# Optimization experiments

Hardware: AMD Instinct MI355X
Metric: run time of the kernel (lower is better)

Reference implementation:

```python
import jax, jax.numpy as jnp
import numpy as np

T = 2048        # flattened tokens (one prefill sequence)
HID = 2048      # hidden_size
NH = 32         # query heads
NKV = 4         # kv heads
HD = 128        # head_dim
THETA = 1000000.0
EPS = 1e-6


def setup_inputs() -> dict:
    key = jax.random.key(0)
    k0, k1, k2 = jax.random.split(key, 3)
    return {
        "positions": jnp.arange(T, dtype=jnp.int32),
        "hidden_states": jax.random.normal(k0, (T, HID), dtype=jnp.float32),
        "w_qkv": jax.random.normal(k1, ((NH + 2 * NKV) * HD, HID), dtype=jnp.float32) * 0.02,
        "w_o": jax.random.normal(k2, (HID, NH * HD), dtype=jnp.float32) * 0.02,
        "q_norm_w": jnp.ones((HD,), dtype=jnp.float32),
        "k_norm_w": jnp.ones((HD,), dtype=jnp.float32),
    }


def _rmsnorm(x, w):
    # per-head RMSNorm over last dim (head_dim), fp32 math
    var = jnp.mean(x * x, axis=-1, keepdims=True)
    return x * jax.lax.rsqrt(var + EPS) * w


def _rope(x, positions):
    # NeoX-style rotary embedding over full head_dim
    d = x.shape[-1]
    inv_freq = 1.0 / (THETA ** (jnp.arange(0, d, 2, dtype=jnp.float32) / d))  # [d/2]
    ang = positions.astype(jnp.float32)[:, None] * inv_freq                   # [T, d/2]
    cos = jnp.cos(ang)[:, None, :]  # [T,1,d/2]
    sin = jnp.sin(ang)[:, None, :]
    x1, x2 = jnp.split(x, 2, axis=-1)
    return jnp.concatenate([x1 * cos - x2 * sin, x2 * cos + x1 * sin], axis=-1)


def reference(positions, hidden_states, w_qkv, w_o, q_norm_w, k_norm_w):
    # fused QKV projection (no bias)
    qkv = hidden_states @ w_qkv.T                       # [T, (NH+2*NKV)*HD]
    q, k, v = jnp.split(qkv, [NH * HD, (NH + NKV) * HD], axis=-1)
    q = _rmsnorm(q.reshape(T, NH, HD), q_norm_w)        # [T,NH,HD]
    k = _rmsnorm(k.reshape(T, NKV, HD), k_norm_w)       # [T,NKV,HD]
    v = v.reshape(T, NKV, HD)
    q = _rope(q, positions)
    k = _rope(k, positions)
    # GQA: expand kv heads to query heads
    g = NH // NKV
    k = jnp.repeat(k, g, axis=1)                        # [T,NH,HD]
    v = jnp.repeat(v, g, axis=1)
    scale = HD ** -0.5
    scores = jnp.einsum('qhd,khd->hqk', q, k) * scale   # [NH,T,T]
    causal = jnp.tril(jnp.ones((T, T), dtype=bool))
    scores = jnp.where(causal[None, :, :], scores, jnp.finfo(scores.dtype).min)
    attn = jax.nn.softmax(scores, axis=-1)
    o = jnp.einsum('hqk,khd->qhd', attn, v).reshape(T, NH * HD)
    return o @ w_o.T                                    # [T,HID]
```

## Files before the change

kernel.cpp:

```cpp
#include <hip/hip_runtime.h>
#include <math.h>

#define T 2048
#define HID 2048
#define NH 32
#define NKV 4
#define HD 128
#define QKV_DIM 5120
#define OD 4096
#define C2LOG 0.12751743f
#define MFIX 6.0f

typedef _Float16 half8 __attribute__((ext_vector_type(8)));
typedef _Float16 half4v __attribute__((ext_vector_type(4)));
typedef float floatx4 __attribute__((ext_vector_type(4)));
typedef float floatx16 __attribute__((ext_vector_type(16)));
typedef unsigned uint4v __attribute__((ext_vector_type(4)));

#define GLD16(gp, lp) __builtin_amdgcn_global_load_lds( \
    (const __attribute__((address_space(1))) void*)(gp), \
    (__attribute__((address_space(3))) void*)(lp), 16, 0, 0)

__device__ __forceinline__ unsigned pk_u32(float a, float b) {
    auto h = __builtin_amdgcn_cvt_pkrtz(a, b);
    return __builtin_bit_cast(unsigned, h);
}
__device__ __forceinline__ void plswap(unsigned &a, unsigned &b) {
    asm("v_permlane32_swap_b32 %0, %1" : "+v"(a), "+v"(b));
}

__global__ __launch_bounds__(256)
void cvt_all(const float* __restrict__ h, const float* __restrict__ wq,
             const float* __restrict__ wo, _Float16* __restrict__ out) {
    size_t i = ((size_t)blockIdx.x * 256 + threadIdx.x) * 4;
    const float* src;
    size_t off;
    if (i < (size_t)T * HID)                        { src = h;  off = i; }
    else if (i < (size_t)T * HID + (size_t)QKV_DIM * HID)
                                                    { src = wq; off = i - (size_t)T * HID; }
    else                                            { src = wo; off = i - (size_t)T * HID - (size_t)QKV_DIM * HID; }
    float4 v = *(const float4*)(src + off);
    half4v o = { (_Float16)v.x, (_Float16)v.y, (_Float16)v.z, (_Float16)v.w };
    *(half4v*)(out + i) = o;
}

__global__ __launch_bounds__(256)
void gemm_sk_h(const _Float16* __restrict__ A, const _Float16* __restrict__ B,
               _Float16* __restrict__ p0, _Float16* __restrict__ p1,
               int M, int N, int K, int KS) {
    __shared__ __align__(16) _Float16 Asm[8192];
    __shared__ __align__(16) _Float16 Bsm[8192];
    int tid = threadIdx.x;
    int wave = tid >> 6, lane = tid & 63;
    int quad = lane >> 4, l16 = lane & 15;
    int m0 = blockIdx.y * 128, n0 = blockIdx.x * 128;
    int koff = blockIdx.z * KS;
    _Float16* C = blockIdx.z ? p1 : p0;
    int wm = (wave >> 1) * 64, wn = (wave & 1) * 64;
    const _Float16* Ag = A + (size_t)(m0 + (tid >> 2)) * K + koff + (tid & 3) * 8;
    const _Float16* Bg = B + (size_t)(n0 + (tid >> 2)) * K + koff + (tid & 3) * 8;
    size_t row64 = (size_t)64 * K;
    int wofs = wave * 512;
    floatx4 acc[4][4] = {};
    int nt = KS >> 5;
    GLD16(Ag, Asm + wofs);
    GLD16(Ag + row64, Asm + 2048 + wofs);
    GLD16(Bg, Bsm + wofs);
    GLD16(Bg + row64, Bsm + 2048 + wofs);
    for (int t = 0; t < nt; t++) {
        int cur = t & 1;
        if (t + 1 < nt) {
            const _Float16* Agp = Ag + (size_t)(t + 1) * 32;
            const _Float16* Bgp = Bg + (size_t)(t + 1) * 32;
            int nb = (cur ^ 1) * 4096 + wofs;
            GLD16(Agp, Asm + nb);
            GLD16(Agp + row64, Asm + nb + 2048);
            GLD16(Bgp, Bsm + nb);
            GLD16(Bgp + row64, Bsm + nb + 2048);
            asm volatile("s_waitcnt vmcnt(4)" ::: "memory");
        } else {
            asm volatile("s_waitcnt vmcnt(0)" ::: "memory");
        }
        __builtin_amdgcn_s_barrier();
        __builtin_amdgcn_sched_barrier(0);
        int pb = cur * 4096;
        half8 af[4], bf[4];
        #pragma unroll
        for (int i = 0; i < 4; i++)
            af[i] = *(const half8*)&Asm[pb + (wm + i * 16 + l16) * 32 + quad * 8];
        #pragma unroll
        for (int j = 0; j < 4; j++)
            bf[j] = *(const half8*)&Bsm[pb + (wn + j * 16 + l16) * 32 + quad * 8];
        #pragma unroll
        for (int i = 0; i < 4; i++)
            #pragma unroll
            for (int j = 0; j < 4; j++)
                acc[i][j] = __builtin_amdgcn_mfma_f32_16x16x32_f16(af[i], bf[j], acc[i][j], 0, 0, 0);
        __builtin_amdgcn_s_barrier();
    }
    #pragma unroll
    for (int i = 0; i < 4; i++) {
        int row = m0 + wm + i * 16 + quad * 4;
        #pragma unroll
        for (int j = 0; j < 4; j++) {
            int col = n0 + wn + j * 16 + l16;
            #pragma unroll
            for (int r = 0; r < 4; r++)
                C[(size_t)(row + r) * N + col] = (_Float16)acc[i][j][r];
        }
    }
}

__global__ __launch_bounds__(256)
void gemm_sk_f(const _Float16* __restrict__ A, const _Float16* __restrict__ B,
               _Float16* __restrict__ p0, _Float16* __restrict__ p1,
               _Float16* __restrict__ p2, _Float16* __restrict__ p3,
               int M, int N, int K, int KS) {
    __shared__ __align__(16) _Float16 Asm[8192];
    __shared__ __align__(16) _Float16 Bsm[8192];
    int tid = threadIdx.x;
    int wave = tid >> 6, lane = tid & 63;
    int quad = lane >> 4, l16 = lane & 15;
    int m0 = blockIdx.y * 128, n0 = blockIdx.x * 128;
    int bz = blockIdx.z;
    int koff = bz * KS;
    _Float16* C = (bz == 0) ? p0 : (bz == 1) ? p1 : (bz == 2) ? p2 : p3;
    int wm = (wave >> 1) * 64, wn = (wave & 1) * 64;
    const _Float16* Ag = A + (size_t)(m0 + (tid >> 2)) * K + koff + (tid & 3) * 8;
    const _Float16* Bg = B + (size_t)(n0 + (tid >> 2)) * K + koff + (tid & 3) * 8;
    size_t row64 = (size_t)64 * K;
    int wofs = wave * 512;
    floatx4 acc[4][4] = {};
    int nt = KS >> 5;
    GLD16(Ag, Asm + wofs);
    GLD16(Ag + row64, Asm + 2048 + wofs);
    GLD16(Bg, Bsm + wofs);
    GLD16(Bg + row64, Bsm + 2048 + wofs);
    for (int t = 0; t < nt; t++) {
        int cur = t & 1;
        if (t + 1 < nt) {
            const _Float16* Agp = Ag + (size_t)(t + 1) * 32;
            const _Float16* Bgp = Bg + (size_t)(t + 1) * 32;
            int nb = (cur ^ 1) * 4096 + wofs;
            GLD16(Agp, Asm + nb);
            GLD16(Agp + row64, Asm + nb + 2048);
            GLD16(Bgp, Bsm + nb);
            GLD16(Bgp + row64, Bsm + nb + 2048);
            asm volatile("s_waitcnt vmcnt(4)" ::: "memory");
        } else {
            asm volatile("s_waitcnt vmcnt(0)" ::: "memory");
        }
        __builtin_amdgcn_s_barrier();
        __builtin_amdgcn_sched_barrier(0);
        int pb = cur * 4096;
        half8 af[4], bf[4];
        #pragma unroll
        for (int i = 0; i < 4; i++)
            af[i] = *(const half8*)&Asm[pb + (wm + i * 16 + l16) * 32 + quad * 8];
        #pragma unroll
        for (int j = 0; j < 4; j++)
            bf[j] = *(const half8*)&Bsm[pb + (wn + j * 16 + l16) * 32 + quad * 8];
        #pragma unroll
        for (int i = 0; i < 4; i++)
            #pragma unroll
            for (int j = 0; j < 4; j++)
                acc[i][j] = __builtin_amdgcn_mfma_f32_16x16x32_f16(af[i], bf[j], acc[i][j], 0, 0, 0);
        __builtin_amdgcn_s_barrier();
    }
    #pragma unroll
    for (int i = 0; i < 4; i++) {
        int row = m0 + wm + i * 16 + quad * 4;
        #pragma unroll
        for (int j = 0; j < 4; j++) {
            int col = n0 + wn + j * 16 + l16;
            #pragma unroll
            for (int r = 0; r < 4; r++)
                C[(size_t)(row + r) * N + col] = (_Float16)acc[i][j][r];
        }
    }
}

__global__ __launch_bounds__(256)
void reduce4(const _Float16* __restrict__ p0, const _Float16* __restrict__ p1,
             const _Float16* __restrict__ p2, const _Float16* __restrict__ p3,
             float* __restrict__ out) {
    size_t i = ((size_t)blockIdx.x * 256 + threadIdx.x) * 4;
    half4v a = *(const half4v*)(p0 + i);
    half4v b = *(const half4v*)(p1 + i);
    half4v c = *(const half4v*)(p2 + i);
    half4v d = *(const half4v*)(p3 + i);
    float4 o = { (float)a.x + (float)b.x + (float)c.x + (float)d.x,
                 (float)a.y + (float)b.y + (float)c.y + (float)d.y,
                 (float)a.z + (float)b.z + (float)c.z + (float)d.z,
                 (float)a.w + (float)b.w + (float)c.w + (float)d.w };
    *(float4*)(out + i) = o;
}

__global__ __launch_bounds__(256)
void qkv_post(const _Float16* __restrict__ qp0, const _Float16* __restrict__ qp1,
              const int* __restrict__ positions,
              const float* __restrict__ qw, const float* __restrict__ kw,
              _Float16* __restrict__ Qb, _Float16* __restrict__ Kb,
              _Float16* __restrict__ Vt) {
    int t = blockIdx.x;
    int wave = threadIdx.x >> 6, lane = threadIdx.x & 63;
    float pos = (float)positions[t];
    float f = exp2f(-(float)lane * (19.9315685693241741f / 64.0f));
    float ang = pos * f;
    float s = sinf(ang), c = cosf(ang);
    const _Float16* r0 = qp0 + (size_t)t * QKV_DIM;
    const _Float16* r1 = qp1 + (size_t)t * QKV_DIM;
    for (int hh = wave; hh < NH + 2 * NKV; hh += 4) {
        float x1 = (float)r0[hh * HD + lane] + (float)r1[hh * HD + lane];
        float x2 = (float)r0[hh * HD + lane + 64] + (float)r1[hh * HD + lane + 64];
        if (hh < NH + NKV) {
            float ss = x1 * x1 + x2 * x2;
            for (int o = 1; o < 64; o <<= 1) ss += __shfl_xor(ss, o);
            float inv = rsqrtf(ss * (1.0f / HD) + 1e-6f);
            const float* w = (hh < NH) ? qw : kw;
            x1 = x1 * inv * w[lane];
            x2 = x2 * inv * w[lane + 64];
            float y1 = x1 * c - x2 * s;
            float y2 = x2 * c + x1 * s;
            _Float16* dst;
            if (hh < NH) dst = Qb + ((size_t)hh * T + t) * HD;
            else         dst = Kb + ((size_t)(hh - NH) * T + t) * HD;
            dst[lane]      = (_Float16)y1;
            dst[lane + 64] = (_Float16)y2;
        } else {
            int hk = hh - NH - NKV;
            Vt[((size_t)hk * HD + lane) * T + t]      = (_Float16)x1;
            Vt[((size_t)hk * HD + lane + 64) * T + t] = (_Float16)x2;
        }
    }
}

__global__ __launch_bounds__(256, 2)
void attn(const _Float16* __restrict__ Qb, const _Float16* __restrict__ Kb,
          const _Float16* __restrict__ Vt, _Float16* __restrict__ Ob) {
    __shared__ __align__(16) _Float16 Ksm[8192];
    __shared__ __align__(16) _Float16 Vsm[8192];
    int b = blockIdx.x;
    int halfg = b >> 8;
    int idx = b & 255;
    int h = idx & 31;
    int qi = idx >> 5;
    int j = halfg ? qi : 15 - qi;
    int hk = h >> 3;
    int tid = threadIdx.x, wave = tid >> 6, lane = tid & 63;
    int l31 = lane & 31, hi = lane >> 5;
    int wq0 = j * 128 + wave * 32;
    int qa = wq0 + l31;

    half8 qf[8];
    {
        const _Float16* qp = Qb + ((size_t)h * T + qa) * HD + hi * 8;
        #pragma unroll
        for (int kb = 0; kb < 8; kb++)
            qf[kb] = *(const half8*)(qp + kb * 16);
    }
    floatx16 o_acc[4] = {};
    float lsum = 0.0f;

    int krow = tid >> 4;
    const _Float16* Kg = Kb + ((size_t)hk * T + krow) * HD + ((tid & 15) ^ (krow & 7)) * 8;
    int vrow = tid >> 3;
    const _Float16* Vg = Vt + ((size_t)hk * HD + vrow) * T + ((tid & 7) ^ (vrow & 7)) * 8;
    _Float16* KsmW = Ksm + wave * 512;
    _Float16* VsmW = Vsm + wave * 512;

    int ntiles = 2 * j + 2;
    for (int it = 0; it < ntiles; it++) {
        int kv0 = it * 64;
        __syncthreads();
        {
            const _Float16* kg = Kg + (size_t)kv0 * HD;
            const _Float16* vg = Vg + kv0;
            #pragma unroll
            for (int c = 0; c < 4; c++) {
                GLD16(kg + (size_t)c * (16 * HD), KsmW + c * 2048);
                GLD16(vg + (size_t)c * (32 * T), VsmW + c * 2048);
            }
        }
        __syncthreads();

        bool needmask = (it >= ntiles - 2);
        half8 af[4];
        #pragma unroll
        for (int s = 0; s < 2; s++) {
            int row = s * 32 + l31;
            int rs = row & 7;
            floatx16 sc = {};
            #pragma unroll
            for (int kb = 0; kb < 8; kb++) {
                half8 kf = *(const half8*)&Ksm[row * 128 + (((kb * 2 + hi) ^ rs)) * 8];
                sc = __builtin_amdgcn_mfma_f32_32x32x16_f16(kf, qf[kb], sc, 0, 0, 0);
            }
            float pe[16];
            #pragma unroll
            for (int r = 0; r < 16; r++) {
                float p = __builtin_amdgcn_exp2f(
                    __builtin_fmaf(sc[r], C2LOG, -MFIX));
                if (needmask) {
                    int kv = kv0 + s * 32 + (r & 3) + 8 * (r >> 2) + 4 * hi;
                    p = (kv <= qa) ? p : 0.0f;
                }
                lsum += p;
                pe[r] = p;
            }
            #pragma unroll
            for (int c = 0; c < 2; c++) {
                int rb = c * 8;
                unsigned x0 = pk_u32(pe[rb + 0], pe[rb + 1]);
                unsigned y0 = pk_u32(pe[rb + 4], pe[rb + 5]);
                plswap(x0, y0);
                unsigned x1 = pk_u32(pe[rb + 2], pe[rb + 3]);
                unsigned y1 = pk_u32(pe[rb + 6], pe[rb + 7]);
                plswap(x1, y1);
                uint4v w = { x0, x1, y0, y1 };
                af[s * 2 + c] = __builtin_bit_cast(half8, w);
            }
        }
        #pragma unroll
        for (int db = 0; db < 4; db++) {
            int row = db * 32 + l31;
            int rs = row & 7;
            #pragma unroll
            for (int c = 0; c < 4; c++) {
                half8 vf = *(const half8*)&Vsm[row * 64 + (((c * 2 + hi) ^ rs)) * 8];
                o_acc[db] = __builtin_amdgcn_mfma_f32_32x32x16_f16(af[c], vf, o_acc[db], 0, 0, 0);
            }
        }
    }

    lsum += __shfl_xor(lsum, 32);
    float linv = 1.0f / lsum;
    float li[16];
    #pragma unroll
    for (int r = 0; r < 16; r++) {
        int rq = (r & 3) + 8 * (r >> 2) + 4 * hi;
        li[r] = __shfl(linv, rq);
    }
    #pragma unroll
    for (int db = 0; db < 4; db++) {
        int col = h * HD + db * 32 + l31;
        #pragma unroll
        for (int r = 0; r < 16; r++) {
            int rq = (r & 3) + 8 * (r >> 2) + 4 * hi;
            Ob[(size_t)(wq0 + rq) * OD + col] = (_Float16)(o_acc[db][r] * li[r]);
        }
    }
}

extern "C" void kernel_launch(void* const* d_in, const int* in_sizes, int n_in,
                              void* d_out, int out_size, void* d_ws, size_t ws_size,
                              hipStream_t stream) {
    const int*   positions = (const int*)d_in[0];
    const float* hidden    = (const float*)d_in[1];
    const float* w_qkv     = (const float*)d_in[2];
    const float* w_o       = (const float*)d_in[3];
    const float* q_norm_w  = (const float*)d_in[4];
    const float* k_norm_w  = (const float*)d_in[5];
    float* out = (float*)d_out;

    const size_t MiB = 1048576;
    char* ws = (char*)d_ws;
    _Float16* hb    = (_Float16*)(ws);
    _Float16* wqkvb = (_Float16*)(ws + 8 * MiB);
    _Float16* wob   = (_Float16*)(ws + 28 * MiB);
    _Float16* qkvp0 = (_Float16*)(ws + 44 * MiB);
    _Float16* qkvp1 = (_Float16*)(ws + 64 * MiB);
    _Float16* Qb    = (_Float16*)(ws + 84 * MiB);
    _Float16* Kb    = (_Float16*)(ws + 100 * MiB);
    _Float16* Vt    = (_Float16*)(ws + 102 * MiB);
    _Float16* Ob    = (_Float16*)(ws + 104 * MiB);
    _Float16* op0   = (_Float16*)(ws);
    _Float16* op1   = (_Float16*)(ws + 9 * MiB);
    _Float16* op2   = (_Float16*)(ws + 44 * MiB);
    _Float16* op3   = (_Float16*)(ws + 53 * MiB);

    cvt_all<<<22528, 256, 0, stream>>>(hidden, w_qkv, w_o, hb);

    gemm_sk_h<<<dim3(QKV_DIM / 128, T / 128, 2), 256, 0, stream>>>(
        hb, wqkvb, qkvp0, qkvp1, T, QKV_DIM, HID, HID / 2);

    qkv_post<<<T, 256, 0, stream>>>(qkvp0, qkvp1, positions, q_norm_w, k_norm_w, Qb, Kb, Vt);

    attn<<<512, 256, 0, stream>>>(Qb, Kb, Vt, Ob);

    gemm_sk_f<<<dim3(HID / 128, T / 128, 4), 256, 0, stream>>>(
        Ob, wob, op0, op1, op2, op3, T, HID, OD, OD / 4);
    reduce4<<<T * HID / 1024, 256, 0, stream>>>(op0, op1, op2, op3, out);
}
```

Measured before the change: 341.2 us.

## Add tiled V transpose kernel and use 2-way split-K for output projection

Moves the V transpose out of qkv_post into a dedicated LDS-tiled kernel, so Vt is written with coalesced 16-byte stores instead of strided scalar stores. The output projection now reuses the 2-way split-K GEMM kernel rather than a 4-way one, which halves the partial buffers written and read by the reduction. Each split-K block therefore loops over twice as many K tiles and the grid has fewer blocks, and the change adds one extra kernel launch.

```diff
diff --git a/kernel.cpp b/kernel.cpp
--- a/kernel.cpp
+++ b/kernel.cpp
@@ -8,6 +8,7 @@
 #define HD 128
 #define QKV_DIM 5120
 #define OD 4096
+#define VOFF 4608
 #define C2LOG 0.12751743f
 #define MFIX 6.0f
 
@@ -112,87 +113,13 @@
 }
 
 __global__ __launch_bounds__(256)
-void gemm_sk_f(const _Float16* __restrict__ A, const _Float16* __restrict__ B,
-               _Float16* __restrict__ p0, _Float16* __restrict__ p1,
-               _Float16* __restrict__ p2, _Float16* __restrict__ p3,
-               int M, int N, int K, int KS) {
-    __shared__ __align__(16) _Float16 Asm[8192];
-    __shared__ __align__(16) _Float16 Bsm[8192];
-    int tid = threadIdx.x;
-    int wave = tid >> 6, lane = tid & 63;
-    int quad = lane >> 4, l16 = lane & 15;
-    int m0 = blockIdx.y * 128, n0 = blockIdx.x * 128;
-    int bz = blockIdx.z;
-    int koff = bz * KS;
-    _Float16* C = (bz == 0) ? p0 : (bz == 1) ? p1 : (bz == 2) ? p2 : p3;
-    int wm = (wave >> 1) * 64, wn = (wave & 1) * 64;
-    const _Float16* Ag = A + (size_t)(m0 + (tid >> 2)) * K + koff + (tid & 3) * 8;
-    const _Float16* Bg = B + (size_t)(n0 + (tid >> 2)) * K + koff + (tid & 3) * 8;
-    size_t row64 = (size_t)64 * K;
-    int wofs = wave * 512;
-    floatx4 acc[4][4] = {};
-    int nt = KS >> 5;
-    GLD16(Ag, Asm + wofs);
-    GLD16(Ag + row64, Asm + 2048 + wofs);
-    GLD16(Bg, Bsm + wofs);
-    GLD16(Bg + row64, Bsm + 2048 + wofs);
-    for (int t = 0; t < nt; t++) {
-        int cur = t & 1;
-        if (t + 1 < nt) {
-            const _Float16* Agp = Ag + (size_t)(t + 1) * 32;
-            const _Float16* Bgp = Bg + (size_t)(t + 1) * 32;
-            int nb = (cur ^ 1) * 4096 + wofs;
-            GLD16(Agp, Asm + nb);
-            GLD16(Agp + row64, Asm + nb + 2048);
-            GLD16(Bgp, Bsm + nb);
-            GLD16(Bgp + row64, Bsm + nb + 2048);
-            asm volatile("s_waitcnt vmcnt(4)" ::: "memory");
-        } else {
-            asm volatile("s_waitcnt vmcnt(0)" ::: "memory");
-        }
-        __builtin_amdgcn_s_barrier();
-        __builtin_amdgcn_sched_barrier(0);
-        int pb = cur * 4096;
-        half8 af[4], bf[4];
-        #pragma unroll
-        for (int i = 0; i < 4; i++)
-            af[i] = *(const half8*)&Asm[pb + (wm + i * 16 + l16) * 32 + quad * 8];
-        #pragma unroll
-        for (int j = 0; j < 4; j++)
-            bf[j] = *(const half8*)&Bsm[pb + (wn + j * 16 + l16) * 32 + quad * 8];
-        #pragma unroll
-        for (int i = 0; i < 4; i++)
-            #pragma unroll
-            for (int j = 0; j < 4; j++)
-                acc[i][j] = __builtin_amdgcn_mfma_f32_16x16x32_f16(af[i], bf[j], acc[i][j], 0, 0, 0);
-        __builtin_amdgcn_s_barrier();
-    }
-    #pragma unroll
-    for (int i = 0; i < 4; i++) {
-        int row = m0 + wm + i * 16 + quad * 4;
-        #pragma unroll
-        for (int j = 0; j < 4; j++) {
-            int col = n0 + wn + j * 16 + l16;
-            #pragma unroll
-            for (int r = 0; r < 4; r++)
-                C[(size_t)(row + r) * N + col] = (_Float16)acc[i][j][r];
-        }
-    }
-}
-
-__global__ __launch_bounds__(256)
-void reduce4(const _Float16* __restrict__ p0, const _Float16* __restrict__ p1,
-             const _Float16* __restrict__ p2, const _Float16* __restrict__ p3,
+void reduce2(const _Float16* __restrict__ p0, const _Float16* __restrict__ p1,
              float* __restrict__ out) {
     size_t i = ((size_t)blockIdx.x * 256 + threadIdx.x) * 4;
     half4v a = *(const half4v*)(p0 + i);
     half4v b = *(const half4v*)(p1 + i);
-    half4v c = *(const half4v*)(p2 + i);
-    half4v d = *(const half4v*)(p3 + i);
-    float4 o = { (float)a.x + (float)b.x + (float)c.x + (float)d.x,
-                 (float)a.y + (float)b.y + (float)c.y + (float)d.y,
-                 (float)a.z + (float)b.z + (float)c.z + (float)d.z,
-                 (float)a.w + (float)b.w + (float)c.w + (float)d.w };
+    float4 o = { (float)a.x + (float)b.x, (float)a.y + (float)b.y,
+                 (float)a.z + (float)b.z, (float)a.w + (float)b.w };
     *(float4*)(out + i) = o;
 }
 
@@ -200,8 +127,7 @@
 void qkv_post(const _Float16* __restrict__ qp0, const _Float16* __restrict__ qp1,
               const int* __restrict__ positions,
               const float* __restrict__ qw, const float* __restrict__ kw,
-              _Float16* __restrict__ Qb, _Float16* __restrict__ Kb,
-              _Float16* __restrict__ Vt) {
+              _Float16* __restrict__ Qb, _Float16* __restrict__ Kb) {
     int t = blockIdx.x;
     int wave = threadIdx.x >> 6, lane = threadIdx.x & 63;
     float pos = (float)positions[t];
@@ -210,28 +136,51 @@
     float s = sinf(ang), c = cosf(ang);
     const _Float16* r0 = qp0 + (size_t)t * QKV_DIM;
     const _Float16* r1 = qp1 + (size_t)t * QKV_DIM;
-    for (int hh = wave; hh < NH + 2 * NKV; hh += 4) {
+    for (int hh = wave; hh < NH + NKV; hh += 4) {
         float x1 = (float)r0[hh * HD + lane] + (float)r1[hh * HD + lane];
         float x2 = (float)r0[hh * HD + lane + 64] + (float)r1[hh * HD + lane + 64];
-        if (hh < NH + NKV) {
-            float ss = x1 * x1 + x2 * x2;
-            for (int o = 1; o < 64; o <<= 1) ss += __shfl_xor(ss, o);
-            float inv = rsqrtf(ss * (1.0f / HD) + 1e-6f);
-            const float* w = (hh < NH) ? qw : kw;
-            x1 = x1 * inv * w[lane];
-            x2 = x2 * inv * w[lane + 64];
-            float y1 = x1 * c - x2 * s;
-            float y2 = x2 * c + x1 * s;
-            _Float16* dst;
-            if (hh < NH) dst = Qb + ((size_t)hh * T + t) * HD;
-            else         dst = Kb + ((size_t)(hh - NH) * T + t) * HD;
-            dst[lane]      = (_Float16)y1;
-            dst[lane + 64] = (_Float16)y2;
-        } else {
-            int hk = hh - NH - NKV;
-            Vt[((size_t)hk * HD + lane) * T + t]      = (_Float16)x1;
-            Vt[((size_t)hk * HD + lane + 64) * T + t] = (_Float16)x2;
-        }
+        float ss = x1 * x1 + x2 * x2;
+        for (int o = 1; o < 64; o <<= 1) ss += __shfl_xor(ss, o);
+        float inv = rsqrtf(ss * (1.0f / HD) + 1e-6f);
+        const float* w = (hh < NH) ? qw : kw;
+        x1 = x1 * inv * w[lane];
+        x2 = x2 * inv * w[lane + 64];
+        float y1 = x1 * c - x2 * s;
+        float y2 = x2 * c + x1 * s;
+        _Float16* dst;
+        if (hh < NH) dst = Qb + ((size_t)hh * T + t) * HD;
+        else         dst = Kb + ((size_t)(hh - NH) * T + t) * HD;
+        dst[lane]      = (_Float16)y1;
+        dst[lane + 64] = (_Float16)y2;
+    }
+}
+
+__global__ __launch_bounds__(256)
+void v_trans(const _Float16* __restrict__ qp0, const _Float16* __restrict__ qp1,
+             _Float16* __restrict__ Vt) {
+    __shared__ _Float16 Ls[64][72];
+    int tz = blockIdx.x & 31, dz = blockIdx.x >> 5;
+    int tid = threadIdx.x;
+    int rr = tid >> 3, c8 = (tid & 7) * 8;
+    #pragma unroll
+    for (int it = 0; it < 2; it++) {
+        int row = it * 32 + rr;
+        size_t src = (size_t)(tz * 64 + row) * QKV_DIM + VOFF + dz * 64 + c8;
+        half8 a = *(const half8*)(qp0 + src);
+        half8 b = *(const half8*)(qp1 + src);
+        half8 sv;
+        #pragma unroll
+        for (int e = 0; e < 8; e++) sv[e] = (_Float16)((float)a[e] + (float)b[e]);
+        *(half8*)&Ls[row][c8] = sv;
+    }
+    __syncthreads();
+    #pragma unroll
+    for (int it = 0; it < 2; it++) {
+        int d = it * 32 + rr;
+        half8 o;
+        #pragma unroll
+        for (int e = 0; e < 8; e++) o[e] = Ls[c8 + e][d];
+        *(half8*)(Vt + (size_t)(dz * 64 + d) * T + tz * 64 + c8) = o;
     }
 }
 
@@ -376,19 +325,18 @@
     _Float16* Ob    = (_Float16*)(ws + 104 * MiB);
     _Float16* op0   = (_Float16*)(ws);
     _Float16* op1   = (_Float16*)(ws + 9 * MiB);
-    _Float16* op2   = (_Float16*)(ws + 44 * MiB);
-    _Float16* op3   = (_Float16*)(ws + 53 * MiB);
 
     cvt_all<<<22528, 256, 0, stream>>>(hidden, w_qkv, w_o, hb);
 
     gemm_sk_h<<<dim3(QKV_DIM / 128, T / 128, 2), 256, 0, stream>>>(
         hb, wqkvb, qkvp0, qkvp1, T, QKV_DIM, HID, HID / 2);
 
-    qkv_post<<<T, 256, 0, stream>>>(qkvp0, qkvp1, positions, q_norm_w, k_norm_w, Qb, Kb, Vt);
+    qkv_post<<<T, 256, 0, stream>>>(qkvp0, qkvp1, positions, q_norm_w, k_norm_w, Qb, Kb);
+    v_trans<<<256, 256, 0, stream>>>(qkvp0, qkvp1, Vt);
 
     attn<<<512, 256, 0, stream>>>(Qb, Kb, Vt, Ob);
 
-    gemm_sk_f<<<dim3(HID / 128, T / 128, 4), 256, 0, stream>>>(
-        Ob, wob, op0, op1, op2, op3, T, HID, OD, OD / 4);
-    reduce4<<<T * HID / 1024, 256, 0, stream>>>(op0, op1, op2, op3, out);
-}
+    gemm_sk_h<<<dim3(HID / 128, T / 128, 2), 256, 0, stream>>>(
+        Ob, wob, op0, op1, T, HID, OD, OD / 2);
+    reduce2<<<T * HID / 1024, 256, 0, stream>>>(op0, op1, out);
+}
```

New measurement: 330.5 us. 1.03x faster.
